# Kernel optimization log

Hardware: AMD Instinct MI355X
Metric: run time of the kernel (lower is better)

The kernel has to match this reference:

```python
import jax, jax.numpy as jnp
import numpy as np

# 5-tap image-gradient filter (cross-correlation taps, as in F.conv2d)
_K5 = (-1.0 / 12.0, 2.0 / 3.0, 0.0, -2.0 / 3.0, 1.0 / 12.0)
ALPHA = BETA = GAMMA = DELTA = 1.0
MASK_COST = 1.0
ENTROPY_WEIGHT = 1.0


def _pen(x):
    return jnp.sqrt(x + 1e-5)


def _filt_w(x):
    # depthwise 1x5 filter along W, padding 2 (matches F.conv2d(x, kernel_gx, padding=(0,2)))
    W = x.shape[-1]
    xp = jnp.pad(x, ((0, 0), (0, 0), (0, 0), (2, 2)))
    out = _K5[0] * xp[..., 0:W]
    for j in range(1, 5):
        out = out + _K5[j] * xp[..., j:j + W]
    return out


def _filt_h(x):
    # depthwise 5x1 filter along H, padding 2
    H = x.shape[-2]
    xp = jnp.pad(x, ((0, 0), (0, 0), (2, 2), (0, 0)))
    out = _K5[0] * xp[..., 0:H, :]
    for j in range(1, 5):
        out = out + _K5[j] * xp[..., j:j + H, :]
    return out


def _warp(img, flow):
    # Bilinear warp: sample img at (x + flow_x, y + flow_y); out-of-range taps contribute 0
    B, C, H, W = img.shape
    xq = jnp.arange(W, dtype=img.dtype)[None, None, :] + flow[:, 0]  # (B,H,W)
    yq = jnp.arange(H, dtype=img.dtype)[None, :, None] + flow[:, 1]
    x0 = jnp.floor(xq)
    y0 = jnp.floor(yq)
    wx1 = xq - x0
    wy1 = yq - y0
    img_flat = img.reshape(B, C, H * W)

    def tap(xi, yi, w):
        valid = (xi >= 0) & (xi <= W - 1) & (yi >= 0) & (yi <= H - 1)
        xc = jnp.clip(xi, 0, W - 1).astype(jnp.int32)
        yc = jnp.clip(yi, 0, H - 1).astype(jnp.int32)
        idx = (yc * W + xc).reshape(B, 1, H * W)
        vals = jnp.take_along_axis(img_flat, jnp.broadcast_to(idx, (B, C, H * W)), axis=2)
        vals = vals.reshape(B, C, H, W)
        return vals * (w * valid.astype(img.dtype))[:, None]

    return (tap(x0, y0, (1 - wx1) * (1 - wy1)) + tap(x0 + 1, y0, wx1 * (1 - wy1))
            + tap(x0, y0 + 1, (1 - wx1) * wy1) + tap(x0 + 1, y0 + 1, wx1 * wy1))


def _border_mask(flow):
    B, _, H, W = flow.shape
    Xp = jnp.arange(W, dtype=flow.dtype)[None, None, :] + flow[:, 0]
    Yp = jnp.arange(H, dtype=flow.dtype)[None, :, None] + flow[:, 1]
    mask_x = jax.nn.sigmoid(Xp + 0.5) * (1.0 - jax.nn.sigmoid(Xp - (W - 0.5)))
    mask_y = jax.nn.sigmoid(Yp + 0.5) * (1.0 - jax.nn.sigmoid(Yp - (H - 0.5)))
    return mask_x * mask_y


def _direction_terms(flow_a, flow_b, img_a, img_b):
    # energy terms for one direction (warping *_b by flow_a)
    mask = _border_mask(flow_a)
    flow_b_warp = _warp(flow_b, flow_a)
    mag = jnp.sum(flow_a ** 2 + flow_b_warp ** 2, axis=1)
    diff = flow_a + flow_b_warp
    occ = 1.0 - jax.nn.sigmoid(jnp.sum(diff ** 2, axis=1) - (0.01 * mag + 0.5))
    mask = mask * occ
    mask_term = MASK_COST * jnp.sum(1.0 - mask, axis=(1, 2)).mean()
    img_b_warp = _warp(img_b, flow_a)
    A = jnp.sum((img_a - img_b_warp) ** 2, axis=1)
    data_term = ALPHA * jnp.sum(_pen(A) * mask, axis=(1, 2)).mean()
    dx = flow_a[..., 1:] - flow_a[..., :-1]
    dy = flow_a[:, :, 1:, :] - flow_a[:, :, :-1, :]
    Bt = (jnp.pad(jnp.sum(dx ** 2, axis=1), ((0, 0), (0, 0), (0, 1)))
          + jnp.pad(jnp.sum(dy ** 2, axis=1), ((0, 0), (0, 1), (0, 0))))
    smooth_term = BETA * jnp.sum(_pen(Bt), axis=(1, 2)).mean()
    Ct = (jnp.sum((_filt_w(img_a) - _filt_w(img_b_warp)) ** 2, axis=1)
          + jnp.sum((_filt_h(img_a) - _filt_h(img_b_warp)) ** 2, axis=1))
    grad_term = GAMMA * jnp.sum(_pen(Ct) * mask, axis=(1, 2)).mean()
    D = jnp.sum(diff ** 2, axis=1)
    fb_part = DELTA * jnp.sum(_pen(D) * mask, axis=(1, 2)).mean()
    return mask_term + data_term + smooth_term + grad_term + fb_part


def _elbo_epe(meanf, log_varf, meanb, log_varb, img1, img2, target, noise_f, noise_b):
    # reparameterized flow samples (Nsamples = 1)
    flowf = meanf + jnp.exp(log_varf / 2.0) * noise_f
    flowb = meanb + jnp.exp(log_varb / 2.0) * noise_b
    energy = (_direction_terms(flowf, flowb, img1, img2)
              + _direction_terms(flowb, flowf, img2, img1))
    entropy = (jnp.sum(log_varf, axis=(1, 2, 3)) / 2
               + jnp.sum(log_varb, axis=(1, 2, 3)) / 2).mean()
    elbo = energy - ENTROPY_WEIGHT * entropy
    epe = jnp.sqrt(jnp.sum((meanf - target) ** 2, axis=1)).mean()
    return elbo, epe


def setup_inputs() -> dict:
    key = jax.random.key(0)
    ks = jax.random.split(key, 9)
    B, H, W = 8, 384, 512
    return {
        "meanf": jax.random.normal(ks[0], (B, 2, H, W), jnp.float32),
        "log_varf": jax.random.normal(ks[1], (B, 2, H, W), jnp.float32),
        "meanb": jax.random.normal(ks[2], (B, 2, H, W), jnp.float32),
        "log_varb": jax.random.normal(ks[3], (B, 2, H, W), jnp.float32),
        "img1": jax.random.uniform(ks[4], (B, 3, H, W), jnp.float32),
        "img2": jax.random.uniform(ks[5], (B, 3, H, W), jnp.float32),
        "target": jax.random.normal(ks[6], (B, 2, H, W), jnp.float32),
        "noise_f": jax.random.normal(ks[7], (B, 2, H, W), jnp.float32),
        "noise_b": jax.random.normal(ks[8], (B, 2, H, W), jnp.float32),
    }


def reference(meanf, log_varf, meanb, log_varb, img1, img2, target, noise_f, noise_b):
    elbo, epe = _elbo_epe(meanf, log_varf, meanb, log_varb, img1, img2, target, noise_f, noise_b)
    return (elbo, epe)
```

## Files before the change

### kernel.cpp

```cpp
#include <hip/hip_runtime.h>
#include <math.h>

#define BATCH 8
#define IH 384
#define IW 512
#define NPIX (IH*IW)
#define BN (BATCH*NPIX)

#define TW 64
#define TH 16
#define RW (TW+4)
#define RH (TH+4)
#define RN (RW*RH)
#define NTX (IW/TW)
#define NTY (IH/TH)
#define NB_DIR (NTX*NTY*BATCH*2)

#define NB_FLOW 1536
#define ENT_OFF NB_DIR
#define EPE_OFF (ENT_OFF + NB_FLOW)
#define PART_FLOATS 8192

__device__ __forceinline__ float frcp_(float x){ return __builtin_amdgcn_rcpf(x); }
__device__ __forceinline__ float fsqrt_(float x){ return __builtin_amdgcn_sqrtf(x); }
__device__ __forceinline__ float sigmoidf_(float x){ return frcp_(1.0f + __expf(-x)); }

__device__ __forceinline__ float block_reduce_sum(float v){
    __shared__ float s[8];
    #pragma unroll
    for (int off=32; off>0; off>>=1) v += __shfl_down(v, off);
    int lane = threadIdx.x & 63, wid = threadIdx.x >> 6;
    if (lane==0) s[wid] = v;
    __syncthreads();
    float t = 0.f;
    if (wid==0){
        int nw = (blockDim.x+63)>>6;
        t = (lane < nw) ? s[lane] : 0.f;
        #pragma unroll
        for (int off=4; off>0; off>>=1) t += __shfl_down(t, off);
    }
    __syncthreads();
    return t;
}

__global__ __launch_bounds__(256)
void flows_kernel(const float* __restrict__ meanf, const float* __restrict__ log_varf,
                  const float* __restrict__ meanb, const float* __restrict__ log_varb,
                  const float* __restrict__ target,
                  const float* __restrict__ noise_f, const float* __restrict__ noise_b,
                  float* __restrict__ flowf, float* __restrict__ flowb,
                  float* __restrict__ part)
{
    int t = blockIdx.x*blockDim.x + threadIdx.x;
    const int NP4 = NPIX/4;
    int b = t / NP4, p4 = t - b*NP4;
    size_t i0 = ((size_t)b*2*NPIX)/4 + p4;
    size_t i1 = i0 + NPIX/4;

    const float4* mf = (const float4*)meanf;  const float4* lf = (const float4*)log_varf;
    const float4* mb = (const float4*)meanb;  const float4* lb = (const float4*)log_varb;
    const float4* nf = (const float4*)noise_f; const float4* nb = (const float4*)noise_b;
    const float4* tg = (const float4*)target;
    float4* ff = (float4*)flowf; float4* fbp = (float4*)flowb;

    float4 lf0 = lf[i0], lf1 = lf[i1], lb0 = lb[i0], lb1 = lb[i1];
    float4 mf0 = mf[i0], mf1 = mf[i1], mb0 = mb[i0], mb1 = mb[i1];
    float4 nf0 = nf[i0], nf1 = nf[i1], nb0 = nb[i0], nb1 = nb[i1];

    float4 o;
    o.x = mf0.x + __expf(0.5f*lf0.x)*nf0.x; o.y = mf0.y + __expf(0.5f*lf0.y)*nf0.y;
    o.z = mf0.z + __expf(0.5f*lf0.z)*nf0.z; o.w = mf0.w + __expf(0.5f*lf0.w)*nf0.w;
    ff[i0] = o;
    o.x = mf1.x + __expf(0.5f*lf1.x)*nf1.x; o.y = mf1.y + __expf(0.5f*lf1.y)*nf1.y;
    o.z = mf1.z + __expf(0.5f*lf1.z)*nf1.z; o.w = mf1.w + __expf(0.5f*lf1.w)*nf1.w;
    ff[i1] = o;
    o.x = mb0.x + __expf(0.5f*lb0.x)*nb0.x; o.y = mb0.y + __expf(0.5f*lb0.y)*nb0.y;
    o.z = mb0.z + __expf(0.5f*lb0.z)*nb0.z; o.w = mb0.w + __expf(0.5f*lb0.w)*nb0.w;
    fbp[i0] = o;
    o.x = mb1.x + __expf(0.5f*lb1.x)*nb1.x; o.y = mb1.y + __expf(0.5f*lb1.y)*nb1.y;
    o.z = mb1.z + __expf(0.5f*lb1.z)*nb1.z; o.w = mb1.w + __expf(0.5f*lb1.w)*nb1.w;
    fbp[i1] = o;

    float ent = (lf0.x+lf0.y+lf0.z+lf0.w) + (lf1.x+lf1.y+lf1.z+lf1.w)
              + (lb0.x+lb0.y+lb0.z+lb0.w) + (lb1.x+lb1.y+lb1.z+lb1.w);

    float4 t0 = tg[i0], t1 = tg[i1];
    float d0, d1, epe = 0.f;
    d0 = mf0.x - t0.x; d1 = mf1.x - t1.x; epe += fsqrt_(d0*d0 + d1*d1);
    d0 = mf0.y - t0.y; d1 = mf1.y - t1.y; epe += fsqrt_(d0*d0 + d1*d1);
    d0 = mf0.z - t0.z; d1 = mf1.z - t1.z; epe += fsqrt_(d0*d0 + d1*d1);
    d0 = mf0.w - t0.w; d1 = mf1.w - t1.w; epe += fsqrt_(d0*d0 + d1*d1);

    float s = block_reduce_sum(ent);
    if (threadIdx.x == 0) part[ENT_OFF + blockIdx.x] = s;
    float s2 = block_reduce_sum(epe);
    if (threadIdx.x == 0) part[EPE_OFF + blockIdx.x] = s2;
}

__global__ __launch_bounds__(256)
void dir_kernel(const float* __restrict__ flowf, const float* __restrict__ flowb,
                const float* __restrict__ img1, const float* __restrict__ img2,
                float* __restrict__ part)
{
    __shared__ float wlds[3][RH][RW];
    __shared__ float mlds[TH][TW];

    const int dir = blockIdx.z & 1, b = blockIdx.z >> 1;
    const float *pfa, *pfb, *pia, *pib;
    if (dir == 0){ pfa = flowf; pfb = flowb; pia = img1; pib = img2; }
    else         { pfa = flowb; pfb = flowf; pia = img2; pib = img1; }
    pfa += (size_t)b*2*NPIX; pfb += (size_t)b*2*NPIX;
    pia += (size_t)b*3*NPIX; pib += (size_t)b*3*NPIX;

    const int tw0 = blockIdx.x*TW, th0 = blockIdx.y*TH;
    const int tid = threadIdx.x;
    float local = 0.f;

    for (int i = tid; i < RN; i += 256){
        int hh = i / RW, ww = i - hh*RW;
        int gh = th0 + hh - 2, gw = tw0 + ww - 2;
        bool inimg = (gh >= 0) && (gh < IH) && (gw >= 0) && (gw < IW);
        float w0 = 0.f, w1 = 0.f, w2 = 0.f;
        if (inimg){
            int p = gh*IW + gw;
            float fax = pfa[p], fay = pfa[NPIX + p];
            float Xp = (float)gw + fax;
            float Yp = (float)gh + fay;

            float x0f = floorf(Xp), y0f = floorf(Yp);
            float wx1 = Xp - x0f, wy1 = Yp - y0f;
            float wx0 = 1.f - wx1, wy0 = 1.f - wy1;
            int idx[4]; float wt[4];
            {
                float xs[4] = {x0f, x0f + 1.f, x0f,       x0f + 1.f};
                float ys[4] = {y0f, y0f,       y0f + 1.f, y0f + 1.f};
                float wsx[4] = {wx0*wy0, wx1*wy0, wx0*wy1, wx1*wy1};
                #pragma unroll
                for (int k = 0; k < 4; ++k){
                    bool valid = (xs[k] >= 0.f) && (xs[k] <= (float)(IW-1)) &&
                                 (ys[k] >= 0.f) && (ys[k] <= (float)(IH-1));
                    float xc = fminf(fmaxf(xs[k], 0.f), (float)(IW-1));
                    float yc = fminf(fmaxf(ys[k], 0.f), (float)(IH-1));
                    idx[k] = (int)yc * IW + (int)xc;
                    wt[k]  = valid ? wsx[k] : 0.f;
                }
            }

            w0 = wt[0]*pib[idx[0]] + wt[1]*pib[idx[1]] + wt[2]*pib[idx[2]] + wt[3]*pib[idx[3]];
            {
                const float* s1 = pib + NPIX;
                const float* s2 = pib + 2*NPIX;
                w1 = wt[0]*s1[idx[0]] + wt[1]*s1[idx[1]] + wt[2]*s1[idx[2]] + wt[3]*s1[idx[3]];
                w2 = wt[0]*s2[idx[0]] + wt[1]*s2[idx[1]] + wt[2]*s2[idx[2]] + wt[3]*s2[idx[3]];
            }

            bool interior = (hh >= 2) && (hh < RH-2) && (ww >= 2) && (ww < RW-2);
            if (interior){
                float mx = sigmoidf_(Xp + 0.5f) * (1.f - sigmoidf_(Xp - ((float)IW - 0.5f)));
                float my = sigmoidf_(Yp + 0.5f) * (1.f - sigmoidf_(Yp - ((float)IH - 0.5f)));
                float bm = mx * my;

                float fbwx = wt[0]*pfb[idx[0]] + wt[1]*pfb[idx[1]] + wt[2]*pfb[idx[2]] + wt[3]*pfb[idx[3]];
                const float* pfb1 = pfb + NPIX;
                float fbwy = wt[0]*pfb1[idx[0]] + wt[1]*pfb1[idx[1]] + wt[2]*pfb1[idx[2]] + wt[3]*pfb1[idx[3]];

                float mag = fax*fax + fay*fay + fbwx*fbwx + fbwy*fbwy;
                float dfx = fax + fbwx, dfy = fay + fbwy;
                float D = dfx*dfx + dfy*dfy;
                float occ = 1.f - sigmoidf_(D - (0.01f*mag + 0.5f));
                float mask = bm * occ;
                mlds[hh-2][ww-2] = mask;

                local += (1.f - mask);

                float d0 = pia[p]        - w0;
                float d1 = pia[NPIX+p]   - w1;
                float d2 = pia[2*NPIX+p] - w2;
                local += fsqrt_(d0*d0 + d1*d1 + d2*d2 + 1e-5f) * mask;

                local += fsqrt_(D + 1e-5f) * mask;

                float Bt = 0.f;
                if (gw < IW-1){
                    float e0 = pfa[p+1] - fax;
                    float e1 = pfa[NPIX + p+1] - fay;
                    Bt += e0*e0 + e1*e1;
                }
                if (gh < IH-1){
                    float e0 = pfa[p+IW] - fax;
                    float e1 = pfa[NPIX + p+IW] - fay;
                    Bt += e0*e0 + e1*e1;
                }
                local += fsqrt_(Bt + 1e-5f);
            }
        }
        wlds[0][hh][ww] = w0;
        wlds[1][hh][ww] = w1;
        wlds[2][hh][ww] = w2;
    }
    __syncthreads();

    const float K0 = -1.f/12.f, K1 = 2.f/3.f, K3 = -2.f/3.f, K4 = 1.f/12.f;
    for (int i = tid; i < TW*TH; i += 256){
        int hh = i >> 6, ww = i & 63;
        int gh = th0 + hh, gw = tw0 + ww;
        int lh = hh + 2, lw = ww + 2;
        int p = gh*IW + gw;
        float Ct = 0.f;
        #pragma unroll
        for (int c = 0; c < 3; ++c){
            const float* A_ = pia + (size_t)c*NPIX;
            float gxa = 0.f;
            if (gw >= 2)    gxa += K0*A_[p-2];
            if (gw >= 1)    gxa += K1*A_[p-1];
            if (gw <= IW-2) gxa += K3*A_[p+1];
            if (gw <= IW-3) gxa += K4*A_[p+2];
            float gxw = K0*wlds[c][lh][lw-2] + K1*wlds[c][lh][lw-1]
                      + K3*wlds[c][lh][lw+1] + K4*wlds[c][lh][lw+2];
            float d = gxa - gxw; Ct += d*d;
            float gya = 0.f;
            if (gh >= 2)    gya += K0*A_[p-2*IW];
            if (gh >= 1)    gya += K1*A_[p-IW];
            if (gh <= IH-2) gya += K3*A_[p+IW];
            if (gh <= IH-3) gya += K4*A_[p+2*IW];
            float gyw = K0*wlds[c][lh-2][lw] + K1*wlds[c][lh-1][lw]
                      + K3*wlds[c][lh+1][lw] + K4*wlds[c][lh+2][lw];
            d = gya - gyw; Ct += d*d;
        }
        local += fsqrt_(Ct + 1e-5f) * mlds[hh][ww];
    }

    float s = block_reduce_sum(local);
    if (tid == 0) part[blockIdx.x + NTX*(blockIdx.y + NTY*blockIdx.z)] = s;
}

__global__ __launch_bounds__(256)
void finalize_kernel(const float* __restrict__ part, float* __restrict__ out)
{
    float e = 0.f, ent = 0.f, epe = 0.f;
    for (int i = threadIdx.x; i < NB_DIR; i += 256) e += part[i];
    for (int i = threadIdx.x; i < NB_FLOW; i += 256){
        ent += part[ENT_OFF + i];
        epe += part[EPE_OFF + i];
    }
    e   = block_reduce_sum(e);
    ent = block_reduce_sum(ent);
    epe = block_reduce_sum(epe);
    if (threadIdx.x == 0){
        out[0] = e / (float)BATCH - ent / (2.f * (float)BATCH);
        out[1] = epe / ((float)BATCH * (float)NPIX);
    }
}

extern "C" void kernel_launch(void* const* d_in, const int* in_sizes, int n_in,
                              void* d_out, int out_size, void* d_ws, size_t ws_size,
                              hipStream_t stream)
{
    const float* meanf    = (const float*)d_in[0];
    const float* log_varf = (const float*)d_in[1];
    const float* meanb    = (const float*)d_in[2];
    const float* log_varb = (const float*)d_in[3];
    const float* img1     = (const float*)d_in[4];
    const float* img2     = (const float*)d_in[5];
    const float* target   = (const float*)d_in[6];
    const float* noise_f  = (const float*)d_in[7];
    const float* noise_b  = (const float*)d_in[8];

    float* ws    = (float*)d_ws;
    float* part  = ws;
    float* flowf = ws + PART_FLOATS;
    float* flowb = flowf + 2*(size_t)BN;

    const int threads = 256;

    flows_kernel<<<NB_FLOW, threads, 0, stream>>>(meanf, log_varf, meanb, log_varb,
                                                  target, noise_f, noise_b,
                                                  flowf, flowb, part);

    dim3 grid(NTX, NTY, BATCH*2);
    dir_kernel<<<grid, threads, 0, stream>>>(flowf, flowb, img1, img2, part);

    finalize_kernel<<<1, threads, 0, stream>>>(part, (float*)d_out);
}
```

Measured before the change: 265.4 us.

## Stage target image window in LDS for bilinear warp gathers

Before the warp loop, each block loads a haloed window (8-pixel border) of the three-channel target image into shared memory using float4 loads. Bilinear taps whose four neighbours fall inside that window read from LDS, and the rest fall back to global gathers. This is meant to replace scattered global gathers with LDS reads, at the cost of an extra staging pass, more shared memory per block (which may lower occupancy) and a divergent fallback branch. Flow inputs are standard normal, so most displacements stay well within the window.

```diff
diff --git a/kernel.cpp b/kernel.cpp
--- a/kernel.cpp
+++ b/kernel.cpp
@@ -15,6 +15,11 @@
 #define NTX (IW/TW)
 #define NTY (IH/TH)
 #define NB_DIR (NTX*NTY*BATCH*2)
+
+#define HS 8
+#define SH (TH+2*HS)
+#define SW (TW+2*HS)
+#define SF4 (SW/4)
 
 #define NB_FLOW 1536
 #define ENT_OFF NB_DIR
@@ -102,6 +107,7 @@
                 const float* __restrict__ img1, const float* __restrict__ img2,
                 float* __restrict__ part)
 {
+    __shared__ float sib[3][SH][SW];
     __shared__ float wlds[3][RH][RW];
     __shared__ float mlds[TH][TW];
 
@@ -115,6 +121,20 @@
     const int tw0 = blockIdx.x*TW, th0 = blockIdx.y*TH;
     const int tid = threadIdx.x;
     float local = 0.f;
+
+    for (int i = tid; i < 3*SH*SF4; i += 256){
+        int c = i / (SH*SF4);
+        int rem = i - c*(SH*SF4);
+        int r = rem / SF4, c4 = rem - r*SF4;
+        int gy = th0 - HS + r;
+        int gx = tw0 - HS + 4*c4;
+        float4 v = make_float4(0.f, 0.f, 0.f, 0.f);
+        if (gy >= 0 && gy < IH && gx >= 0 && gx < IW){
+            v = *(const float4*)(pib + (size_t)c*NPIX + gy*IW + gx);
+        }
+        *(float4*)&sib[c][r][4*c4] = v;
+    }
+    __syncthreads();
 
     for (int i = tid; i < RN; i += 256){
         int hh = i / RW, ww = i - hh*RW;
@@ -130,28 +150,42 @@
             float x0f = floorf(Xp), y0f = floorf(Yp);
             float wx1 = Xp - x0f, wy1 = Yp - y0f;
             float wx0 = 1.f - wx1, wy0 = 1.f - wy1;
-            int idx[4]; float wt[4];
-            {
-                float xs[4] = {x0f, x0f + 1.f, x0f,       x0f + 1.f};
-                float ys[4] = {y0f, y0f,       y0f + 1.f, y0f + 1.f};
-                float wsx[4] = {wx0*wy0, wx1*wy0, wx0*wy1, wx1*wy1};
-                #pragma unroll
-                for (int k = 0; k < 4; ++k){
-                    bool valid = (xs[k] >= 0.f) && (xs[k] <= (float)(IW-1)) &&
-                                 (ys[k] >= 0.f) && (ys[k] <= (float)(IH-1));
-                    float xc = fminf(fmaxf(xs[k], 0.f), (float)(IW-1));
-                    float yc = fminf(fmaxf(ys[k], 0.f), (float)(IH-1));
-                    idx[k] = (int)yc * IW + (int)xc;
-                    wt[k]  = valid ? wsx[k] : 0.f;
-                }
-            }
-
-            w0 = wt[0]*pib[idx[0]] + wt[1]*pib[idx[1]] + wt[2]*pib[idx[2]] + wt[3]*pib[idx[3]];
-            {
-                const float* s1 = pib + NPIX;
-                const float* s2 = pib + 2*NPIX;
-                w1 = wt[0]*s1[idx[0]] + wt[1]*s1[idx[1]] + wt[2]*s1[idx[2]] + wt[3]*s1[idx[3]];
-                w2 = wt[0]*s2[idx[0]] + wt[1]*s2[idx[1]] + wt[2]*s2[idx[2]] + wt[3]*s2[idx[3]];
+
+            float x1f = x0f + 1.f, y1f = y0f + 1.f;
+            bool vx0 = (x0f >= 0.f) && (x0f <= (float)(IW-1));
+            bool vx1 = (x1f >= 0.f) && (x1f <= (float)(IW-1));
+            bool vy0 = (y0f >= 0.f) && (y0f <= (float)(IH-1));
+            bool vy1 = (y1f >= 0.f) && (y1f <= (float)(IH-1));
+            float xc0 = fminf(fmaxf(x0f, 0.f), (float)(IW-1));
+            float xc1 = fminf(fmaxf(x1f, 0.f), (float)(IW-1));
+            float yc0 = fminf(fmaxf(y0f, 0.f), (float)(IH-1));
+            float yc1 = fminf(fmaxf(y1f, 0.f), (float)(IH-1));
+            int ix0 = (int)xc0, ix1 = (int)xc1, iy0 = (int)yc0, iy1 = (int)yc1;
+            int idx0 = iy0*IW + ix0, idx1 = iy0*IW + ix1;
+            int idx2 = iy1*IW + ix0, idx3 = iy1*IW + ix1;
+            float wt0 = (vx0 && vy0) ? wx0*wy0 : 0.f;
+            float wt1 = (vx1 && vy0) ? wx1*wy0 : 0.f;
+            float wt2 = (vx0 && vy1) ? wx0*wy1 : 0.f;
+            float wt3 = (vx1 && vy1) ? wx1*wy1 : 0.f;
+
+            int lx0 = ix0 - (tw0 - HS), ly0 = iy0 - (th0 - HS);
+            int lx1 = ix1 - (tw0 - HS), ly1 = iy1 - (th0 - HS);
+            bool inwin = (lx0 >= 0) && (lx1 < SW) && (ly0 >= 0) && (ly1 < SH);
+            if (inwin){
+                int o00 = ly0*SW + lx0, o01 = ly0*SW + lx1;
+                int o10 = ly1*SW + lx0, o11 = ly1*SW + lx1;
+                const float* s0 = &sib[0][0][0];
+                const float* s1 = s0 + SH*SW;
+                const float* s2 = s1 + SH*SW;
+                w0 = wt0*s0[o00] + wt1*s0[o01] + wt2*s0[o10] + wt3*s0[o11];
+                w1 = wt0*s1[o00] + wt1*s1[o01] + wt2*s1[o10] + wt3*s1[o11];
+                w2 = wt0*s2[o00] + wt1*s2[o01] + wt2*s2[o10] + wt3*s2[o11];
+            } else {
+                const float* g1 = pib + NPIX;
+                const float* g2 = pib + 2*NPIX;
+                w0 = wt0*pib[idx0] + wt1*pib[idx1] + wt2*pib[idx2] + wt3*pib[idx3];
+                w1 = wt0*g1[idx0]  + wt1*g1[idx1]  + wt2*g1[idx2]  + wt3*g1[idx3];
+                w2 = wt0*g2[idx0]  + wt1*g2[idx1]  + wt2*g2[idx2]  + wt3*g2[idx3];
             }
 
             bool interior = (hh >= 2) && (hh < RH-2) && (ww >= 2) && (ww < RW-2);
@@ -160,9 +194,9 @@
                 float my = sigmoidf_(Yp + 0.5f) * (1.f - sigmoidf_(Yp - ((float)IH - 0.5f)));
                 float bm = mx * my;
 
-                float fbwx = wt[0]*pfb[idx[0]] + wt[1]*pfb[idx[1]] + wt[2]*pfb[idx[2]] + wt[3]*pfb[idx[3]];
+                float fbwx = wt0*pfb[idx0] + wt1*pfb[idx1] + wt2*pfb[idx2] + wt3*pfb[idx3];
                 const float* pfb1 = pfb + NPIX;
-                float fbwy = wt[0]*pfb1[idx[0]] + wt[1]*pfb1[idx[1]] + wt[2]*pfb1[idx[2]] + wt[3]*pfb1[idx[3]];
+                float fbwy = wt0*pfb1[idx0] + wt1*pfb1[idx1] + wt2*pfb1[idx2] + wt3*pfb1[idx3];
 
                 float mag = fax*fax + fay*fay + fbwx*fbwx + fbwy*fbwy;
                 float dfx = fax + fbwx, dfy = fay + fbwy;
```

After: 274.1 us. 1.03x slower.
